# Kernel optimization log

Measured on AMD Instinct MI355X. Metric: run time of the kernel, lower is better.

The kernel has to match this reference:

```python
import jax, jax.numpy as jnp
import numpy as np

IN_DIM, HID, D_PK = 6, 64, 64
B, T = 256, 2048
EPS = 1e-5


def setup_inputs() -> dict:
    key = jax.random.key(0)
    ks = jax.random.split(key, 12)
    s_in = 1.0 / np.sqrt(IN_DIM)
    s_h = 1.0 / np.sqrt(HID)
    return {
        "drug_ce": jax.random.normal(ks[0], (B, T, IN_DIM), dtype=jnp.float32),
        "w1": jax.random.uniform(ks[1], (IN_DIM, HID), minval=-s_in, maxval=s_in, dtype=jnp.float32),
        "b1": jax.random.uniform(ks[2], (HID,), minval=-s_in, maxval=s_in, dtype=jnp.float32),
        "ln1_g": jnp.ones((HID,), jnp.float32),
        "ln1_b": jnp.zeros((HID,), jnp.float32),
        "W_ih": jax.random.uniform(ks[3], (3 * HID, HID), minval=-s_h, maxval=s_h, dtype=jnp.float32),
        "b_ih": jax.random.uniform(ks[4], (3 * HID,), minval=-s_h, maxval=s_h, dtype=jnp.float32),
        "W_hh": jax.random.uniform(ks[5], (3 * HID, HID), minval=-s_h, maxval=s_h, dtype=jnp.float32),
        "b_hh": jax.random.uniform(ks[6], (3 * HID,), minval=-s_h, maxval=s_h, dtype=jnp.float32),
        "w2": jax.random.uniform(ks[7], (HID, D_PK), minval=-s_h, maxval=s_h, dtype=jnp.float32),
        "b2": jax.random.uniform(ks[8], (D_PK,), minval=-s_h, maxval=s_h, dtype=jnp.float32),
        "ln2_g": jnp.ones((D_PK,), jnp.float32),
        "ln2_b": jnp.zeros((D_PK,), jnp.float32),
    }


def _layernorm(x, g, b):
    m = jnp.mean(x, axis=-1, keepdims=True)
    v = jnp.mean(jnp.square(x - m), axis=-1, keepdims=True)
    return (x - m) * jax.lax.rsqrt(v + EPS) * g + b


def reference(drug_ce, w1, b1, ln1_g, ln1_b, W_ih, b_ih, W_hh, b_hh, w2, b2, ln2_g, ln2_b):
    # input_proj: Linear -> LayerNorm -> GELU (exact, erf-based as in torch)
    x = jax.nn.gelu(_layernorm(drug_ce @ w1 + b1, ln1_g, ln1_b), approximate=False)  # (B,T,H)

    # Precompute input-side gate pre-activations for all timesteps
    gi = jnp.einsum('bth,gh->btg', x, W_ih) + b_ih  # (B,T,3H)
    gi_t = jnp.swapaxes(gi, 0, 1)  # (T,B,3H)

    h0 = jnp.zeros((drug_ce.shape[0], HID), dtype=drug_ce.dtype)

    def step(h, gi_step):
        gh = h @ W_hh.T + b_hh  # (B,3H)
        i_r, i_z, i_n = jnp.split(gi_step, 3, axis=-1)
        h_r, h_z, h_n = jnp.split(gh, 3, axis=-1)
        r = jax.nn.sigmoid(i_r + h_r)
        z = jax.nn.sigmoid(i_z + h_z)
        n = jnp.tanh(i_n + r * h_n)
        h_new = (1.0 - z) * n + z * h
        return h_new, h_new

    _, h_seq_t = jax.lax.scan(step, h0, gi_t)  # (T,B,H)
    h_seq = jnp.swapaxes(h_seq_t, 0, 1)  # (B,T,H)

    # out_proj: Linear -> LayerNorm
    return _layernorm(h_seq @ w2 + b2, ln2_g, ln2_b)
```

## Files before the change

kernel.cpp:

```cpp
#include <hip/hip_runtime.h>
#include <math.h>

#define HID 64
#define TST 2048
#define CH 16
#define NCH (TST / CH)
#define EPSN 1e-5f

typedef float v2f __attribute__((ext_vector_type(2)));

__global__ void k_inproj(const float* __restrict__ ce, const float* __restrict__ w1,
                         const float* __restrict__ b1, const float* __restrict__ g1,
                         const float* __restrict__ be1, float* __restrict__ xout,
                         int nrows) {
    const int lane = threadIdx.x & 63;
    const int wave = threadIdx.x >> 6;
    const long row = (long)blockIdx.x * 4 + wave;
    if (row >= nrows) return;
    const float* cr = ce + row * 6;
    float acc = b1[lane];
    acc += cr[0] * w1[0 * HID + lane];
    acc += cr[1] * w1[1 * HID + lane];
    acc += cr[2] * w1[2 * HID + lane];
    acc += cr[3] * w1[3 * HID + lane];
    acc += cr[4] * w1[4 * HID + lane];
    acc += cr[5] * w1[5 * HID + lane];
    float s = acc;
#pragma unroll
    for (int m = 32; m >= 1; m >>= 1) s += __shfl_xor(s, m, 64);
    const float mean = s * (1.0f / 64.0f);
    const float d = acc - mean;
    float q = d * d;
#pragma unroll
    for (int m = 32; m >= 1; m >>= 1) q += __shfl_xor(q, m, 64);
    const float var = q * (1.0f / 64.0f);
    const float xn = d * rsqrtf(var + EPSN) * g1[lane] + be1[lane];
    const float ge = 0.5f * xn * (1.0f + erff(xn * 0.70710678118654752440f));
    xout[row * HID + lane] = ge;
}

__global__ __launch_bounds__(256, 1)
__attribute__((amdgpu_waves_per_eu(1, 1)))
void k_gru(float* xo,
           const float* __restrict__ W_ih, const float* __restrict__ b_ih,
           const float* __restrict__ W_hh, const float* __restrict__ b_hh,
           const float* __restrict__ w2, const float* __restrict__ b2,
           const float* __restrict__ g2, const float* __restrict__ be2) {
    __shared__ __align__(16) float4 xbuf[2][CH][16];
    __shared__ __align__(16) float gibuf[2][CH][192];
    __shared__ __align__(16) float hist[2][CH][HID];
    __shared__ __align__(16) float hbuf[HID];

    const int tid = threadIdx.x;
    const int lane = tid & 63;
    const int wv = tid >> 6;
    float* xb = xo + (size_t)blockIdx.x * TST * HID;

    v2f wr[32], wz[32], wn[32];
    float bhr = 0.f, bhz = 0.f, bhn = 0.f;
    v2f wiA[32], wiB[32];
    float biA = 0.f, biB = 0.f;
    v2f w2v[32];
    float b2r = 0.f, g2r = 0.f, be2r = 0.f;

    if (wv == 0) {
        const v2f* r0 = (const v2f*)(W_hh + (size_t)lane * HID);
        const v2f* r1 = (const v2f*)(W_hh + (size_t)(64 + lane) * HID);
        const v2f* r2 = (const v2f*)(W_hh + (size_t)(128 + lane) * HID);
#pragma unroll
        for (int k = 0; k < 32; ++k) { wr[k] = r0[k]; wz[k] = r1[k]; wn[k] = r2[k]; }
        bhr = b_hh[lane]; bhz = b_hh[64 + lane]; bhn = b_hh[128 + lane];
        hbuf[lane] = 0.0f;
    } else if (wv == 1) {
        const v2f* rA = (const v2f*)(W_ih + (size_t)lane * HID);
        const v2f* rB = (const v2f*)(W_ih + (size_t)(128 + lane) * HID);
#pragma unroll
        for (int k = 0; k < 32; ++k) { wiA[k] = rA[k]; wiB[k] = rB[k]; }
        biA = b_ih[lane]; biB = b_ih[128 + lane];
    } else if (wv == 2) {
        const v2f* rA = (const v2f*)(W_ih + (size_t)(64 + lane) * HID);
#pragma unroll
        for (int k = 0; k < 32; ++k) { wiA[k] = rA[k]; }
        biA = b_ih[64 + lane];
    } else {
#pragma unroll
        for (int k = 0; k < 32; ++k) {
            w2v[k].x = w2[(size_t)(2 * k) * HID + lane];
            w2v[k].y = w2[(size_t)(2 * k + 1) * HID + lane];
        }
        b2r = b2[lane]; g2r = g2[lane]; be2r = be2[lane];
    }

    {
        const float4* src = (const float4*)xb;
        ((float4*)xbuf[0])[tid] = src[tid];
    }
    float h_reg = 0.0f;
    __syncthreads();

    for (int p = 0; p <= NCH + 1; ++p) {
        if (wv == 0) {
            if (p >= 1 && p <= NCH) {
                const int c = p - 1;
                const float* gp = (const float*)gibuf[c & 1];
                float* hp = (float*)hist[c & 1];
                for (int t = 0; t < CH; ++t) {
                    const float gr = gp[t * 192 + lane];
                    const float gz = gp[t * 192 + 64 + lane];
                    const float gn = gp[t * 192 + 128 + lane];
                    const v2f* hv = (const v2f*)hbuf;
                    v2f ar = {0.f, 0.f}, az = {0.f, 0.f}, an = {0.f, 0.f};
#pragma unroll
                    for (int k = 0; k < 32; ++k) {
                        const v2f h2 = hv[k];
                        ar += wr[k] * h2;
                        az += wz[k] * h2;
                        an += wn[k] * h2;
                    }
                    const float rpre = gr + ar.x + ar.y + bhr;
                    const float zpre = gz + az.x + az.y + bhz;
                    const float hn = an.x + an.y + bhn;
                    const float r = 1.0f / (1.0f + __expf(-rpre));
                    const float z = 1.0f / (1.0f + __expf(-zpre));
                    const float pre = gn + r * hn;
                    const float e2 = __expf(2.0f * pre);
                    const float n = 1.0f - 2.0f / (e2 + 1.0f);
                    h_reg = (1.0f - z) * n + z * h_reg;
                    hbuf[lane] = h_reg;
                    hp[t * HID + lane] = h_reg;
                }
            }
        } else if (wv == 1 || wv == 2) {
            if (p < NCH) {
                const float4* xc = (const float4*)xbuf[p & 1];
                float* gp = (float*)gibuf[p & 1];
                for (int t = 0; t < CH; ++t) {
                    const v2f* xv = (const v2f*)(xc + t * 16);
                    v2f aA = {0.f, 0.f}, aB = {0.f, 0.f};
                    if (wv == 1) {
#pragma unroll
                        for (int k = 0; k < 32; ++k) {
                            const v2f x2 = xv[k];
                            aA += wiA[k] * x2;
                            aB += wiB[k] * x2;
                        }
                        gp[t * 192 + lane] = aA.x + aA.y + biA;
                        gp[t * 192 + 128 + lane] = aB.x + aB.y + biB;
                    } else {
#pragma unroll
                        for (int k = 0; k < 32; ++k) {
                            const v2f x2 = xv[k];
                            aA += wiA[k] * x2;
                        }
                        gp[t * 192 + 64 + lane] = aA.x + aA.y + biA;
                    }
                }
            }
        } else {
            if (p >= 2) {
                const int ce = p - 2;
                const float* hp = (const float*)hist[ce & 1];
                float yv[CH];
#pragma unroll
                for (int t = 0; t < CH; ++t) {
                    const v2f* hr = (const v2f*)(hp + t * HID);
                    v2f a2 = {0.f, 0.f};
#pragma unroll
                    for (int k = 0; k < 32; ++k) a2 += w2v[k] * hr[k];
                    yv[t] = b2r + a2.x + a2.y;
                }
                float sv[CH], qv[CH];
#pragma unroll
                for (int t = 0; t < CH; ++t) { sv[t] = yv[t]; qv[t] = yv[t] * yv[t]; }
#pragma unroll
                for (int m = 32; m >= 1; m >>= 1) {
#pragma unroll
                    for (int t = 0; t < CH; ++t) sv[t] += __shfl_xor(sv[t], m, 64);
#pragma unroll
                    for (int t = 0; t < CH; ++t) qv[t] += __shfl_xor(qv[t], m, 64);
                }
#pragma unroll
                for (int t = 0; t < CH; ++t) {
                    const float mean = sv[t] * (1.0f / 64.0f);
                    const float var = qv[t] * (1.0f / 64.0f) - mean * mean;
                    const float dd = yv[t] - mean;
                    xb[(size_t)(ce * CH + t) * HID + lane] =
                        dd * rsqrtf(var + EPSN) * g2r + be2r;
                }
            }
            if (p + 1 < NCH) {
                const float4* src = (const float4*)(xb + (size_t)(p + 1) * CH * HID);
                float4* dst = (float4*)xbuf[(p + 1) & 1];
#pragma unroll
                for (int q2 = 0; q2 < 4; ++q2) dst[lane + q2 * 64] = src[lane + q2 * 64];
            }
        }
        __syncthreads();
    }
}

extern "C" void kernel_launch(void* const* d_in, const int* in_sizes, int n_in,
                              void* d_out, int out_size, void* d_ws, size_t ws_size,
                              hipStream_t stream) {
    const float* ce  = (const float*)d_in[0];
    const float* w1  = (const float*)d_in[1];
    const float* b1  = (const float*)d_in[2];
    const float* g1  = (const float*)d_in[3];
    const float* be1 = (const float*)d_in[4];
    const float* Wih = (const float*)d_in[5];
    const float* bih = (const float*)d_in[6];
    const float* Whh = (const float*)d_in[7];
    const float* bhh = (const float*)d_in[8];
    const float* w2  = (const float*)d_in[9];
    const float* b2  = (const float*)d_in[10];
    const float* g2  = (const float*)d_in[11];
    const float* be2 = (const float*)d_in[12];
    float* out = (float*)d_out;

    const int nrows = in_sizes[0] / 6;
    const int B = nrows / TST;

    k_inproj<<<(nrows + 3) / 4, 256, 0, stream>>>(ce, w1, b1, g1, be1, out, nrows);
    k_gru<<<B, 256, 0, stream>>>(out, Wih, bih, Whh, bhh, w2, b2, g2, be2);
}
```

Baseline: 1.990 ms.

## Fuse input projection into GRU kernel and broadcast hidden state via readlane

Removes the separate input-projection kernel and computes Linear+LayerNorm+GELU inside the GRU block. Raw 6-wide inputs are staged through LDS, which avoids writing and re-reading the 64-wide intermediate x in global memory. The recurrence wave now keeps the full W_hh rows as scalars and broadcasts h with readlane instead of round-tripping it through an LDS buffer every timestep. The trade-offs are a deeper four-stage pipeline, more register pressure in wave 0, and 64 serialized readlane operations per step.

```diff
diff --git a/kernel.cpp b/kernel.cpp
--- a/kernel.cpp
+++ b/kernel.cpp
@@ -9,79 +9,62 @@
 
 typedef float v2f __attribute__((ext_vector_type(2)));
 
-__global__ void k_inproj(const float* __restrict__ ce, const float* __restrict__ w1,
-                         const float* __restrict__ b1, const float* __restrict__ g1,
-                         const float* __restrict__ be1, float* __restrict__ xout,
-                         int nrows) {
-    const int lane = threadIdx.x & 63;
-    const int wave = threadIdx.x >> 6;
-    const long row = (long)blockIdx.x * 4 + wave;
-    if (row >= nrows) return;
-    const float* cr = ce + row * 6;
-    float acc = b1[lane];
-    acc += cr[0] * w1[0 * HID + lane];
-    acc += cr[1] * w1[1 * HID + lane];
-    acc += cr[2] * w1[2 * HID + lane];
-    acc += cr[3] * w1[3 * HID + lane];
-    acc += cr[4] * w1[4 * HID + lane];
-    acc += cr[5] * w1[5 * HID + lane];
-    float s = acc;
-#pragma unroll
-    for (int m = 32; m >= 1; m >>= 1) s += __shfl_xor(s, m, 64);
-    const float mean = s * (1.0f / 64.0f);
-    const float d = acc - mean;
-    float q = d * d;
-#pragma unroll
-    for (int m = 32; m >= 1; m >>= 1) q += __shfl_xor(q, m, 64);
-    const float var = q * (1.0f / 64.0f);
-    const float xn = d * rsqrtf(var + EPSN) * g1[lane] + be1[lane];
-    const float ge = 0.5f * xn * (1.0f + erff(xn * 0.70710678118654752440f));
-    xout[row * HID + lane] = ge;
+__device__ __forceinline__ float bcast(float v, int k) {
+    return __int_as_float(__builtin_amdgcn_readlane(__float_as_int(v), k));
 }
 
 __global__ __launch_bounds__(256, 1)
 __attribute__((amdgpu_waves_per_eu(1, 1)))
-void k_gru(float* xo,
-           const float* __restrict__ W_ih, const float* __restrict__ b_ih,
-           const float* __restrict__ W_hh, const float* __restrict__ b_hh,
-           const float* __restrict__ w2, const float* __restrict__ b2,
-           const float* __restrict__ g2, const float* __restrict__ be2) {
-    __shared__ __align__(16) float4 xbuf[2][CH][16];
-    __shared__ __align__(16) float gibuf[2][CH][192];
+void k_fused(const float* __restrict__ ce,
+             const float* __restrict__ w1, const float* __restrict__ b1,
+             const float* __restrict__ g1, const float* __restrict__ be1,
+             const float* __restrict__ W_ih, const float* __restrict__ b_ih,
+             const float* __restrict__ W_hh, const float* __restrict__ b_hh,
+             const float* __restrict__ w2, const float* __restrict__ b2,
+             const float* __restrict__ g2, const float* __restrict__ be2,
+             float* __restrict__ out) {
+    __shared__ float2 cebuf[2][CH * 3];
+    __shared__ __align__(16) float xbuf[2][CH][HID];
+    __shared__ __align__(16) float gibuf[2][3][CH][HID];
     __shared__ __align__(16) float hist[2][CH][HID];
-    __shared__ __align__(16) float hbuf[HID];
 
     const int tid = threadIdx.x;
     const int lane = tid & 63;
     const int wv = tid >> 6;
-    float* xb = xo + (size_t)blockIdx.x * TST * HID;
-
-    v2f wr[32], wz[32], wn[32];
+    const float* ceb = ce + (size_t)blockIdx.x * TST * 6;
+    float* ob = out + (size_t)blockIdx.x * TST * HID;
+
+    float whr[HID], whz[HID], whn[HID];
     float bhr = 0.f, bhz = 0.f, bhn = 0.f;
     v2f wiA[32], wiB[32];
     float biA = 0.f, biB = 0.f;
+    float w1c[6], b1r = 0.f, g1r = 0.f, be1r = 0.f;
     v2f w2v[32];
     float b2r = 0.f, g2r = 0.f, be2r = 0.f;
 
     if (wv == 0) {
-        const v2f* r0 = (const v2f*)(W_hh + (size_t)lane * HID);
-        const v2f* r1 = (const v2f*)(W_hh + (size_t)(64 + lane) * HID);
-        const v2f* r2 = (const v2f*)(W_hh + (size_t)(128 + lane) * HID);
-#pragma unroll
-        for (int k = 0; k < 32; ++k) { wr[k] = r0[k]; wz[k] = r1[k]; wn[k] = r2[k]; }
+#pragma unroll
+        for (int k = 0; k < HID; ++k) {
+            whr[k] = W_hh[(size_t)lane * HID + k];
+            whz[k] = W_hh[(size_t)(64 + lane) * HID + k];
+            whn[k] = W_hh[(size_t)(128 + lane) * HID + k];
+        }
         bhr = b_hh[lane]; bhz = b_hh[64 + lane]; bhn = b_hh[128 + lane];
-        hbuf[lane] = 0.0f;
-    } else if (wv == 1) {
-        const v2f* rA = (const v2f*)(W_ih + (size_t)lane * HID);
-        const v2f* rB = (const v2f*)(W_ih + (size_t)(128 + lane) * HID);
-#pragma unroll
-        for (int k = 0; k < 32; ++k) { wiA[k] = rA[k]; wiB[k] = rB[k]; }
-        biA = b_ih[lane]; biB = b_ih[128 + lane];
-    } else if (wv == 2) {
-        const v2f* rA = (const v2f*)(W_ih + (size_t)(64 + lane) * HID);
-#pragma unroll
-        for (int k = 0; k < 32; ++k) { wiA[k] = rA[k]; }
-        biA = b_ih[64 + lane];
+    } else if (wv == 1 || wv == 2) {
+        const int rA = (wv == 1) ? lane : (128 + lane);
+        const v2f* pA = (const v2f*)(W_ih + (size_t)rA * HID);
+#pragma unroll
+        for (int k = 0; k < 32; ++k) wiA[k] = pA[k];
+        biA = b_ih[rA];
+        if (wv == 1) {
+            const v2f* pB = (const v2f*)(W_ih + (size_t)(64 + lane) * HID);
+#pragma unroll
+            for (int k = 0; k < 32; ++k) wiB[k] = pB[k];
+            biB = b_ih[64 + lane];
+        }
+#pragma unroll
+        for (int i = 0; i < 6; ++i) w1c[i] = w1[i * HID + lane];
+        b1r = b1[lane]; g1r = g1[lane]; be1r = be1[lane];
     } else {
 #pragma unroll
         for (int k = 0; k < 32; ++k) {
@@ -91,75 +74,99 @@
         b2r = b2[lane]; g2r = g2[lane]; be2r = be2[lane];
     }
 
-    {
-        const float4* src = (const float4*)xb;
-        ((float4*)xbuf[0])[tid] = src[tid];
-    }
+    if (tid < 48) cebuf[0][tid] = ((const float2*)ceb)[tid];
     float h_reg = 0.0f;
     __syncthreads();
 
-    for (int p = 0; p <= NCH + 1; ++p) {
+    for (int p = 0; p <= NCH + 2; ++p) {
         if (wv == 0) {
-            if (p >= 1 && p <= NCH) {
-                const int c = p - 1;
-                const float* gp = (const float*)gibuf[c & 1];
-                float* hp = (float*)hist[c & 1];
-                for (int t = 0; t < CH; ++t) {
-                    const float gr = gp[t * 192 + lane];
-                    const float gz = gp[t * 192 + 64 + lane];
-                    const float gn = gp[t * 192 + 128 + lane];
-                    const v2f* hv = (const v2f*)hbuf;
-                    v2f ar = {0.f, 0.f}, az = {0.f, 0.f}, an = {0.f, 0.f};
-#pragma unroll
-                    for (int k = 0; k < 32; ++k) {
-                        const v2f h2 = hv[k];
-                        ar += wr[k] * h2;
-                        az += wz[k] * h2;
-                        an += wn[k] * h2;
+            if (p >= 2 && p <= NCH + 1) {
+                const int c = p - 2;
+                const float* gp = &gibuf[c & 1][0][0][0];
+                float* hp = &hist[c & 1][0][0];
+                for (int t = 0; t < CH; ++t) {
+                    const float gr = gp[0 * CH * HID + t * HID + lane];
+                    const float gz = gp[1 * CH * HID + t * HID + lane];
+                    const float gn = gp[2 * CH * HID + t * HID + lane];
+                    float ar = 0.f, az = 0.f, an = 0.f;
+#pragma unroll
+                    for (int k = 0; k < HID; ++k) {
+                        const float hk = bcast(h_reg, k);
+                        ar = fmaf(whr[k], hk, ar);
+                        az = fmaf(whz[k], hk, az);
+                        an = fmaf(whn[k], hk, an);
                     }
-                    const float rpre = gr + ar.x + ar.y + bhr;
-                    const float zpre = gz + az.x + az.y + bhz;
-                    const float hn = an.x + an.y + bhn;
-                    const float r = 1.0f / (1.0f + __expf(-rpre));
-                    const float z = 1.0f / (1.0f + __expf(-zpre));
-                    const float pre = gn + r * hn;
+                    const float r = 1.0f / (1.0f + __expf(-(gr + ar + bhr)));
+                    const float z = 1.0f / (1.0f + __expf(-(gz + az + bhz)));
+                    const float pre = gn + r * (an + bhn);
                     const float e2 = __expf(2.0f * pre);
                     const float n = 1.0f - 2.0f / (e2 + 1.0f);
                     h_reg = (1.0f - z) * n + z * h_reg;
-                    hbuf[lane] = h_reg;
                     hp[t * HID + lane] = h_reg;
                 }
             }
         } else if (wv == 1 || wv == 2) {
             if (p < NCH) {
-                const float4* xc = (const float4*)xbuf[p & 1];
-                float* gp = (float*)gibuf[p & 1];
-                for (int t = 0; t < CH; ++t) {
-                    const v2f* xv = (const v2f*)(xc + t * 16);
-                    v2f aA = {0.f, 0.f}, aB = {0.f, 0.f};
+                const float2* cb = cebuf[p & 1];
+                const int base = (wv - 1) * 8;
+                float acc[8];
+#pragma unroll
+                for (int i = 0; i < 8; ++i) {
+                    const int row = base + i;
+                    const float2 a = cb[row * 3 + 0];
+                    const float2 bb = cb[row * 3 + 1];
+                    const float2 cc = cb[row * 3 + 2];
+                    acc[i] = b1r + a.x * w1c[0] + a.y * w1c[1] + bb.x * w1c[2] +
+                             bb.y * w1c[3] + cc.x * w1c[4] + cc.y * w1c[5];
+                }
+                float sv[8], qv[8];
+#pragma unroll
+                for (int i = 0; i < 8; ++i) { sv[i] = acc[i]; qv[i] = acc[i] * acc[i]; }
+#pragma unroll
+                for (int m = 32; m >= 1; m >>= 1) {
+#pragma unroll
+                    for (int i = 0; i < 8; ++i) sv[i] += __shfl_xor(sv[i], m, 64);
+#pragma unroll
+                    for (int i = 0; i < 8; ++i) qv[i] += __shfl_xor(qv[i], m, 64);
+                }
+#pragma unroll
+                for (int i = 0; i < 8; ++i) {
+                    const float mean = sv[i] * (1.0f / 64.0f);
+                    const float var = qv[i] * (1.0f / 64.0f) - mean * mean;
+                    const float xn = (acc[i] - mean) * rsqrtf(var + EPSN) * g1r + be1r;
+                    xbuf[p & 1][base + i][lane] =
+                        0.5f * xn * (1.0f + erff(xn * 0.70710678118654752440f));
+                }
+            }
+            if (p >= 1 && p <= NCH) {
+                const int c = p - 1;
+                for (int t = 0; t < CH; ++t) {
+                    const v2f* xv = (const v2f*)xbuf[c & 1][t];
                     if (wv == 1) {
+                        v2f aR = {0.f, 0.f}, aZ = {0.f, 0.f};
 #pragma unroll
                         for (int k = 0; k < 32; ++k) {
-                            const v2f x2 = xv[k];
-                            aA += wiA[k] * x2;
-                            aB += wiB[k] * x2;
+                            const v2f xx = xv[k];
+                            aR += wiA[k] * xx;
+                            aZ += wiB[k] * xx;
                         }
-                        gp[t * 192 + lane] = aA.x + aA.y + biA;
-                        gp[t * 192 + 128 + lane] = aB.x + aB.y + biB;
+                        gibuf[c & 1][0][t][lane] = aR.x + aR.y + biA;
+                        gibuf[c & 1][1][t][lane] = aZ.x + aZ.y + biB;
                     } else {
-#pragma unroll
-                        for (int k = 0; k < 32; ++k) {
-                            const v2f x2 = xv[k];
-                            aA += wiA[k] * x2;
-                        }
-                        gp[t * 192 + 64 + lane] = aA.x + aA.y + biA;
+                        v2f aN = {0.f, 0.f};
+#pragma unroll
+                        for (int k = 0; k < 32; ++k) aN += wiA[k] * xv[k];
+                        gibuf[c & 1][2][t][lane] = aN.x + aN.y + biA;
                     }
                 }
             }
         } else {
-            if (p >= 2) {
-                const int ce = p - 2;
-                const float* hp = (const float*)hist[ce & 1];
+            if (p + 1 < NCH && lane < 48)
+                cebuf[(p + 1) & 1][lane] =
+                    ((const float2*)(ceb + (size_t)(p + 1) * CH * 6))[lane];
+            if (p >= 3) {
+                const int c = p - 3;
+                const float* hp = &hist[c & 1][0][0];
                 float yv[CH];
 #pragma unroll
                 for (int t = 0; t < CH; ++t) {
@@ -184,15 +191,9 @@
                     const float mean = sv[t] * (1.0f / 64.0f);
                     const float var = qv[t] * (1.0f / 64.0f) - mean * mean;
                     const float dd = yv[t] - mean;
-                    xb[(size_t)(ce * CH + t) * HID + lane] =
+                    ob[(size_t)(c * CH + t) * HID + lane] =
                         dd * rsqrtf(var + EPSN) * g2r + be2r;
                 }
-            }
-            if (p + 1 < NCH) {
-                const float4* src = (const float4*)(xb + (size_t)(p + 1) * CH * HID);
-                float4* dst = (float4*)xbuf[(p + 1) & 1];
-#pragma unroll
-                for (int q2 = 0; q2 < 4; ++q2) dst[lane + q2 * 64] = src[lane + q2 * 64];
             }
         }
         __syncthreads();
@@ -217,9 +218,8 @@
     const float* be2 = (const float*)d_in[12];
     float* out = (float*)d_out;
 
-    const int nrows = in_sizes[0] / 6;
-    const int B = nrows / TST;
-
-    k_inproj<<<(nrows + 3) / 4, 256, 0, stream>>>(ce, w1, b1, g1, be1, out, nrows);
-    k_gru<<<B, 256, 0, stream>>>(out, Wih, bih, Whh, bhh, w2, b2, g2, be2);
+    const int B = (in_sizes[0] / 6) / TST;
+
+    k_fused<<<B, 256, 0, stream>>>(ce, w1, b1, g1, be1, Wih, bih, Whh, bhh,
+                                   w2, b2, g2, be2, out);
 }
```

Measured after the change: 2.078 ms. 4.4% more time.
